# Performance work log

Measured on AMD Instinct MI355X. Metric: run time of the kernel, lower is better.

Reference implementation:

```python
import jax, jax.numpy as jnp
import numpy as np

B, T, I, H, C = 8192, 28, 28, 128, 10


def setup_inputs() -> dict:
    key = jax.random.key(0)
    ks = jax.random.split(key, 7)
    s_ih = 1.0 / np.sqrt(H)
    return {
        "x": jax.random.normal(ks[0], (B, T, I), dtype=jnp.float32),
        "W_ih": jax.random.normal(ks[1], (4 * H, I), dtype=jnp.float32) * s_ih,
        "W_hh": jax.random.normal(ks[2], (4 * H, H), dtype=jnp.float32) * s_ih,
        "b_ih": jax.random.normal(ks[3], (4 * H,), dtype=jnp.float32) * s_ih,
        "b_hh": jax.random.normal(ks[4], (4 * H,), dtype=jnp.float32) * s_ih,
        "W_fc": jax.random.normal(ks[5], (C, H), dtype=jnp.float32) * s_ih,
        "b_fc": jnp.zeros((C,), dtype=jnp.float32),
    }


def reference(x, W_ih, W_hh, b_ih, b_hh, W_fc, b_fc):
    # x: [B, T, I]. PyTorch LSTM gate order: i, f, g, o.
    b = b_ih + b_hh  # [4H]
    # Precompute input projections for all timesteps: [T, B, 4H]
    x_proj = jnp.einsum("bti,gi->tbg", x, W_ih) + b
    h0 = jnp.zeros((x.shape[0], H), dtype=x.dtype)
    c0 = jnp.zeros_like(h0)

    def step(carry, xp_t):
        h, c = carry
        gates = xp_t + h @ W_hh.T  # [B, 4H]
        i_g, f_g, g_g, o_g = jnp.split(gates, 4, axis=-1)
        i_g = jax.nn.sigmoid(i_g)
        f_g = jax.nn.sigmoid(f_g)
        g_g = jnp.tanh(g_g)
        o_g = jax.nn.sigmoid(o_g)
        c = f_g * c + i_g * g_g
        h = o_g * jnp.tanh(c)
        return (h, c), None

    (h_last, _), _ = jax.lax.scan(step, (h0, c0), x_proj)
    # outputs[:, -1, :] == final hidden state; fc + relu
    return jax.nn.relu(h_last @ W_fc.T + b_fc)
```

## Files before the change

### kernel.cpp

```cpp
#include <hip/hip_runtime.h>
#include <math.h>

typedef __attribute__((ext_vector_type(8)))  _Float16 half8;
typedef __attribute__((ext_vector_type(4)))  _Float16 half4;
typedef __attribute__((ext_vector_type(16))) float    f32x16;

#define TSTEPS 28
#define IDIM   28
#define HDIM   128
#define NCH    10
#define TILE_B 32
#define CDIM   10

#if __has_builtin(__builtin_amdgcn_exp2f)
#define EXP2F(x) __builtin_amdgcn_exp2f(x)
#else
#define EXP2F(x) exp2f(x)
#endif
#if __has_builtin(__builtin_amdgcn_rcpf)
#define RCPF(x) __builtin_amdgcn_rcpf(x)
#else
#define RCPF(x) (1.0f / (x))
#endif

__global__ __launch_bounds__(256) void pack_w(const float* __restrict__ Wih,
                                              const float* __restrict__ Whh,
                                              _Float16* __restrict__ P) {
    int e = blockIdx.x * 256 + threadIdx.x;
    if (e >= NCH * 16 * 64 * 8) return;
    int j  = e & 7;
    int ln = (e >> 3) & 63;
    int ct = (e >> 9) & 15;
    int kc = e >> 13;
    int k   = kc * 16 + ((ln >> 5) << 3) + j;
    int col = ct * 32 + (ln & 31);
    int tt = col >> 7, uu = col & 127;
    float v = 0.f;
    if (k < HDIM)              v = Whh[(tt * HDIM + uu) * HDIM + k];
    else if (k < HDIM + IDIM)  v = Wih[(tt * HDIM + uu) * IDIM + (k - HDIM)];
    P[e] = (_Float16)v;
}

__global__ __launch_bounds__(256, 1) void lstm_kernel(
    const float* __restrict__ x,
    const _Float16* __restrict__ P,
    const float* __restrict__ b_ih, const float* __restrict__ b_hh,
    const float* __restrict__ Wfc,
    const float* __restrict__ b_fc,
    float* __restrict__ out)
{
    __shared__ __align__(16) _Float16 frag[NCH][64][8];
    __shared__ __align__(16) float hplain[TILE_B][132];

    const int tid = threadIdx.x;
    const int l   = tid & 63;
    const int w   = tid >> 6;
    const int b0  = blockIdx.x * TILE_B;
    const int u   = w * 32 + (l & 31);

    half8 breg[4][NCH];
    {
        const half8* Pp = (const half8*)P;
        #pragma unroll
        for (int t4 = 0; t4 < 4; ++t4)
            #pragma unroll
            for (int kc = 0; kc < NCH; ++kc)
                breg[t4][kc] = Pp[(kc * 16 + (t4 * 4 + w)) * 64 + l];
    }
    float biasv[4];
    #pragma unroll
    for (int t4 = 0; t4 < 4; ++t4)
        biasv[t4] = b_ih[t4 * HDIM + u] + b_hh[t4 * HDIM + u];

    {
        float4 z = {0.f, 0.f, 0.f, 0.f};
        ((float4*)frag)[tid]       = z;
        ((float4*)frag)[tid + 256] = z;
        if (tid < 32) {
            int slot = (32 + tid) ^ (((32 + tid) >> 4) & 2);
            float2 z2 = {0.f, 0.f};
            *((float2*)&frag[9][slot][4]) = z2;
        }
    }
    if (tid < 224) {
        int row = tid / 7, xg = tid % 7, xi = xg * 4;
        const float4* xs = (const float4*)(x + ((size_t)(b0 + row) * TSTEPS + 0) * IDIM);
        float4 xv = xs[xg];
        half4 hv = {(_Float16)xv.x, (_Float16)xv.y, (_Float16)xv.z, (_Float16)xv.w};
        int lp = row + 32 * ((xi >> 3) & 1);
        int slot = lp ^ ((lp >> 4) & 2);
        *((half4*)&frag[8 + (xi >> 4)][slot][xi & 7]) = hv;
    }

    float cst[16];
    #pragma unroll
    for (int r = 0; r < 16; ++r) cst[r] = 0.f;

    const int sl = l ^ ((l >> 4) & 2);

    __syncthreads();

    for (int t = 0; t < TSTEPS; ++t) {
        f32x16 acc[4];
        #pragma unroll
        for (int t4 = 0; t4 < 4; ++t4)
            #pragma unroll
            for (int r = 0; r < 16; ++r) acc[t4][r] = biasv[t4];

        #pragma unroll
        for (int kc = 0; kc < NCH; ++kc) {
            half8 a = *((const half8*)&frag[kc][sl][0]);
            acc[0] = __builtin_amdgcn_mfma_f32_32x32x16_f16(a, breg[0][kc], acc[0], 0, 0, 0);
            acc[1] = __builtin_amdgcn_mfma_f32_32x32x16_f16(a, breg[1][kc], acc[1], 0, 0, 0);
            acc[2] = __builtin_amdgcn_mfma_f32_32x32x16_f16(a, breg[2][kc], acc[2], 0, 0, 0);
            acc[3] = __builtin_amdgcn_mfma_f32_32x32x16_f16(a, breg[3][kc], acc[3], 0, 0, 0);
        }
        __syncthreads();

        const int kc_h = u >> 4;
        const int lpb  = 32 * ((l >> 3) & 1);
        const int jh   = l & 7;
        #pragma unroll
        for (int r = 0; r < 16; ++r) {
            float ig = acc[0][r], fg = acc[1][r], gg = acc[2][r], og = acc[3][r];
            float is = RCPF(1.f + EXP2F(ig * -1.44269504f));
            float fs = RCPF(1.f + EXP2F(fg * -1.44269504f));
            float os = RCPF(1.f + EXP2F(og * -1.44269504f));
            float gt = 1.f - 2.f * RCPF(1.f + EXP2F(gg * 2.88539008f));
            float c  = fs * cst[r] + is * gt;
            cst[r] = c;
            float tc = 1.f - 2.f * RCPF(1.f + EXP2F(c * 2.88539008f));
            float h  = os * tc;
            int m  = (r & 3) + 8 * (r >> 2) + 4 * (l >> 5);
            int lp = m + lpb;
            int slot = lp ^ ((lp >> 4) & 2);
            frag[kc_h][slot][jh] = (_Float16)h;
            if (t == TSTEPS - 1) hplain[m][u] = h;
        }
        if (t + 1 < TSTEPS && tid < 224) {
            int row = tid / 7, xg = tid % 7, xi = xg * 4;
            const float4* xs = (const float4*)(x + ((size_t)(b0 + row) * TSTEPS + (t + 1)) * IDIM);
            float4 xv = xs[xg];
            half4 hv = {(_Float16)xv.x, (_Float16)xv.y, (_Float16)xv.z, (_Float16)xv.w};
            int lp = row + 32 * ((xi >> 3) & 1);
            int slot = lp ^ ((lp >> 4) & 2);
            *((half4*)&frag[8 + (xi >> 4)][slot][xi & 7]) = hv;
        }
        __syncthreads();
    }

    for (int idx = tid; idx < TILE_B * CDIM; idx += 256) {
        int row = idx / CDIM, c = idx % CDIM;
        const float4* hv = (const float4*)&hplain[row][0];
        const float4* wf = (const float4*)(Wfc + c * HDIM);
        float s = b_fc[c];
        #pragma unroll
        for (int q = 0; q < 32; ++q) {
            float4 a = hv[q], b = wf[q];
            s += a.x * b.x + a.y * b.y + a.z * b.z + a.w * b.w;
        }
        out[(size_t)(b0 + row) * CDIM + c] = fmaxf(s, 0.f);
    }
}

extern "C" void kernel_launch(void* const* d_in, const int* in_sizes, int n_in,
                              void* d_out, int out_size, void* d_ws, size_t ws_size,
                              hipStream_t stream) {
    const float* x   = (const float*)d_in[0];
    const float* Wih = (const float*)d_in[1];
    const float* Whh = (const float*)d_in[2];
    const float* bih = (const float*)d_in[3];
    const float* bhh = (const float*)d_in[4];
    const float* Wfc = (const float*)d_in[5];
    const float* bfc = (const float*)d_in[6];
    float* out = (float*)d_out;
    _Float16* P = (_Float16*)d_ws;

    hipLaunchKernelGGL(pack_w, dim3(320), dim3(256), 0, stream, Wih, Whh, P);
    hipLaunchKernelGGL(lstm_kernel, dim3(8192 / TILE_B), dim3(256), 0, stream,
                       x, P, bih, bhh, Wfc, bfc, out);
}
```

Baseline: 148.8 us.

## Switch LSTM to 16x16x32 MFMA, 16-row tiles, 512 threads with LDS-resident input weights

The batch tile shrinks from 32 to 16 rows and the block grows from 4 to 8 waves, each wave owning 16 hidden units through 16x16x32 MFMAs. This cuts per-thread weight registers and doubles the grid to 512 blocks, so more blocks can run at once. The input-projection weight chunk is moved into LDS, and the next timestep's x load is issued before the MFMAs so its latency is hidden. The cost is more LDS traffic per step, more blocks re-reading the packed weights, and two block barriers per step across twice as many waves.

```diff
diff --git a/kernel.cpp b/kernel.cpp
--- a/kernel.cpp
+++ b/kernel.cpp
@@ -1,15 +1,15 @@
 #include <hip/hip_runtime.h>
 #include <math.h>
 
-typedef __attribute__((ext_vector_type(8)))  _Float16 half8;
-typedef __attribute__((ext_vector_type(4)))  _Float16 half4;
-typedef __attribute__((ext_vector_type(16))) float    f32x16;
+typedef __attribute__((ext_vector_type(8))) _Float16 half8;
+typedef __attribute__((ext_vector_type(4))) _Float16 half4;
+typedef __attribute__((ext_vector_type(4))) float    f32x4;
 
 #define TSTEPS 28
 #define IDIM   28
 #define HDIM   128
-#define NCH    10
-#define TILE_B 32
+#define NKC    5
+#define TILE_B 16
 #define CDIM   10
 
 #if __has_builtin(__builtin_amdgcn_exp2f)
@@ -27,21 +27,22 @@
                                               const float* __restrict__ Whh,
                                               _Float16* __restrict__ P) {
     int e = blockIdx.x * 256 + threadIdx.x;
-    if (e >= NCH * 16 * 64 * 8) return;
+    if (e >= NKC * 4 * 8 * 64 * 8) return;
     int j  = e & 7;
     int ln = (e >> 3) & 63;
-    int ct = (e >> 9) & 15;
-    int kc = e >> 13;
-    int k   = kc * 16 + ((ln >> 5) << 3) + j;
-    int col = ct * 32 + (ln & 31);
-    int tt = col >> 7, uu = col & 127;
+    int w  = (e >> 9) & 7;
+    int t  = (e >> 12) & 3;
+    int kc = e >> 14;
+    int k  = kc * 32 + ((ln >> 4) << 3) + j;
+    int u  = w * 16 + (ln & 15);
+    int g  = t * HDIM + u;
     float v = 0.f;
-    if (k < HDIM)              v = Whh[(tt * HDIM + uu) * HDIM + k];
-    else if (k < HDIM + IDIM)  v = Wih[(tt * HDIM + uu) * IDIM + (k - HDIM)];
+    if (k < HDIM)              v = Whh[g * HDIM + k];
+    else if (k < HDIM + IDIM)  v = Wih[g * IDIM + (k - HDIM)];
     P[e] = (_Float16)v;
 }
 
-__global__ __launch_bounds__(256, 1) void lstm_kernel(
+__global__ __launch_bounds__(512, 4) void lstm_kernel(
     const float* __restrict__ x,
     const _Float16* __restrict__ P,
     const float* __restrict__ b_ih, const float* __restrict__ b_hh,
@@ -49,23 +50,31 @@
     const float* __restrict__ b_fc,
     float* __restrict__ out)
 {
-    __shared__ __align__(16) _Float16 frag[NCH][64][8];
-    __shared__ __align__(16) float hplain[TILE_B][132];
+    __shared__ __align__(16) _Float16 frag[NKC][64][8];
+    __shared__ __align__(16) _Float16 Plds[4][8][64][8];
+    __shared__ __align__(16) float hplain[TILE_B][HDIM + 4];
 
     const int tid = threadIdx.x;
     const int l   = tid & 63;
     const int w   = tid >> 6;
     const int b0  = blockIdx.x * TILE_B;
-    const int u   = w * 32 + (l & 31);
+    const int u   = w * 16 + (l & 15);
 
-    half8 breg[4][NCH];
+    {
+        const float4* P4 = (const float4*)P;
+        float4* dst = (float4*)Plds;
+        #pragma unroll
+        for (int q = 0; q < 4; ++q)
+            dst[tid + q * 512] = P4[8192 + tid + q * 512];
+    }
+    half8 breg[4][4];
     {
         const half8* Pp = (const half8*)P;
         #pragma unroll
-        for (int t4 = 0; t4 < 4; ++t4)
+        for (int kc = 0; kc < 4; ++kc)
             #pragma unroll
-            for (int kc = 0; kc < NCH; ++kc)
-                breg[t4][kc] = Pp[(kc * 16 + (t4 * 4 + w)) * 64 + l];
+            for (int t4 = 0; t4 < 4; ++t4)
+                breg[t4][kc] = Pp[((kc * 4 + t4) * 8 + w) * 64 + l];
     }
     float biasv[4];
     #pragma unroll
@@ -74,54 +83,60 @@
 
     {
         float4 z = {0.f, 0.f, 0.f, 0.f};
-        ((float4*)frag)[tid]       = z;
-        ((float4*)frag)[tid + 256] = z;
-        if (tid < 32) {
-            int slot = (32 + tid) ^ (((32 + tid) >> 4) & 2);
-            float2 z2 = {0.f, 0.f};
-            *((float2*)&frag[9][slot][4]) = z2;
+        ((float4*)frag)[tid] = z;
+        if (tid < 16) {
+            half4 zh = {(_Float16)0.f, (_Float16)0.f, (_Float16)0.f, (_Float16)0.f};
+            *(half4*)&frag[4][48 + tid][4] = zh;
         }
     }
-    if (tid < 224) {
-        int row = tid / 7, xg = tid % 7, xi = xg * 4;
-        const float4* xs = (const float4*)(x + ((size_t)(b0 + row) * TSTEPS + 0) * IDIM);
-        float4 xv = xs[xg];
+    const int xrow = tid / 7, xg = tid % 7;
+    if (tid < 112) {
+        float4 xv = ((const float4*)(x + ((size_t)(b0 + xrow) * TSTEPS + 0) * IDIM))[xg];
         half4 hv = {(_Float16)xv.x, (_Float16)xv.y, (_Float16)xv.z, (_Float16)xv.w};
-        int lp = row + 32 * ((xi >> 3) & 1);
-        int slot = lp ^ ((lp >> 4) & 2);
-        *((half4*)&frag[8 + (xi >> 4)][slot][xi & 7]) = hv;
+        *(half4*)&frag[4][xrow + 16 * (xg >> 1)][(xg & 1) * 4] = hv;
     }
 
-    float cst[16];
-    #pragma unroll
-    for (int r = 0; r < 16; ++r) cst[r] = 0.f;
-
-    const int sl = l ^ ((l >> 4) & 2);
+    float cst[4] = {0.f, 0.f, 0.f, 0.f};
+    const int kc_h = w >> 1;
+    const int quad = (2 * w + ((l >> 3) & 1)) & 3;
+    const int jh   = l & 7;
 
     __syncthreads();
 
     for (int t = 0; t < TSTEPS; ++t) {
-        f32x16 acc[4];
+        float4 xv;
+        const bool doload = (t + 1 < TSTEPS) && (tid < 112);
+        if (doload)
+            xv = ((const float4*)(x + ((size_t)(b0 + xrow) * TSTEPS + (t + 1)) * IDIM))[xg];
+
+        f32x4 acc[4];
         #pragma unroll
-        for (int t4 = 0; t4 < 4; ++t4)
-            #pragma unroll
-            for (int r = 0; r < 16; ++r) acc[t4][r] = biasv[t4];
+        for (int t4 = 0; t4 < 4; ++t4) {
+            f32x4 a4 = {biasv[t4], biasv[t4], biasv[t4], biasv[t4]};
+            acc[t4] = a4;
+        }
 
         #pragma unroll
-        for (int kc = 0; kc < NCH; ++kc) {
-            half8 a = *((const half8*)&frag[kc][sl][0]);
-            acc[0] = __builtin_amdgcn_mfma_f32_32x32x16_f16(a, breg[0][kc], acc[0], 0, 0, 0);
-            acc[1] = __builtin_amdgcn_mfma_f32_32x32x16_f16(a, breg[1][kc], acc[1], 0, 0, 0);
-            acc[2] = __builtin_amdgcn_mfma_f32_32x32x16_f16(a, breg[2][kc], acc[2], 0, 0, 0);
-            acc[3] = __builtin_amdgcn_mfma_f32_32x32x16_f16(a, breg[3][kc], acc[3], 0, 0, 0);
+        for (int kc = 0; kc < NKC; ++kc) {
+            half8 a = *(const half8*)&frag[kc][l][0];
+            if (kc < 4) {
+                acc[0] = __builtin_amdgcn_mfma_f32_16x16x32_f16(a, breg[0][kc], acc[0], 0, 0, 0);
+                acc[1] = __builtin_amdgcn_mfma_f32_16x16x32_f16(a, breg[1][kc], acc[1], 0, 0, 0);
+                acc[2] = __builtin_amdgcn_mfma_f32_16x16x32_f16(a, breg[2][kc], acc[2], 0, 0, 0);
+                acc[3] = __builtin_amdgcn_mfma_f32_16x16x32_f16(a, breg[3][kc], acc[3], 0, 0, 0);
+            } else {
+                #pragma unroll
+                for (int t4 = 0; t4 < 4; ++t4) {
+                    half8 b = *(const half8*)&Plds[t4][w][l][0];
+                    acc[t4] = __builtin_amdgcn_mfma_f32_16x16x32_f16(a, b, acc[t4], 0, 0, 0);
+                }
+            }
         }
         __syncthreads();
 
-        const int kc_h = u >> 4;
-        const int lpb  = 32 * ((l >> 3) & 1);
-        const int jh   = l & 7;
         #pragma unroll
-        for (int r = 0; r < 16; ++r) {
+        for (int r = 0; r < 4; ++r) {
+            int m = ((l >> 4) << 2) + r;
             float ig = acc[0][r], fg = acc[1][r], gg = acc[2][r], og = acc[3][r];
             float is = RCPF(1.f + EXP2F(ig * -1.44269504f));
             float fs = RCPF(1.f + EXP2F(fg * -1.44269504f));
@@ -131,26 +146,18 @@
             cst[r] = c;
             float tc = 1.f - 2.f * RCPF(1.f + EXP2F(c * 2.88539008f));
             float h  = os * tc;
-            int m  = (r & 3) + 8 * (r >> 2) + 4 * (l >> 5);
-            int lp = m + lpb;
-            int slot = lp ^ ((lp >> 4) & 2);
-            frag[kc_h][slot][jh] = (_Float16)h;
+            frag[kc_h][m + 16 * quad][jh] = (_Float16)h;
             if (t == TSTEPS - 1) hplain[m][u] = h;
         }
-        if (t + 1 < TSTEPS && tid < 224) {
-            int row = tid / 7, xg = tid % 7, xi = xg * 4;
-            const float4* xs = (const float4*)(x + ((size_t)(b0 + row) * TSTEPS + (t + 1)) * IDIM);
-            float4 xv = xs[xg];
+        if (doload) {
             half4 hv = {(_Float16)xv.x, (_Float16)xv.y, (_Float16)xv.z, (_Float16)xv.w};
-            int lp = row + 32 * ((xi >> 3) & 1);
-            int slot = lp ^ ((lp >> 4) & 2);
-            *((half4*)&frag[8 + (xi >> 4)][slot][xi & 7]) = hv;
+            *(half4*)&frag[4][xrow + 16 * (xg >> 1)][(xg & 1) * 4] = hv;
         }
         __syncthreads();
     }
 
-    for (int idx = tid; idx < TILE_B * CDIM; idx += 256) {
-        int row = idx / CDIM, c = idx % CDIM;
+    if (tid < TILE_B * CDIM) {
+        int row = tid / CDIM, c = tid % CDIM;
         const float4* hv = (const float4*)&hplain[row][0];
         const float4* wf = (const float4*)(Wfc + c * HDIM);
         float s = b_fc[c];
@@ -177,6 +184,6 @@
     _Float16* P = (_Float16*)d_ws;
 
     hipLaunchKernelGGL(pack_w, dim3(320), dim3(256), 0, stream, Wih, Whh, P);
-    hipLaunchKernelGGL(lstm_kernel, dim3(8192 / TILE_B), dim3(256), 0, stream,
+    hipLaunchKernelGGL(lstm_kernel, dim3(8192 / TILE_B), dim3(512), 0, stream,
                        x, P, bih, bhh, Wfc, bfc, out);
 }
```

Result: faster. 132.4 us (-11.1%).
